# Optimization experiments

Measured on AMD Instinct MI355X. Metric: run time of the kernel, lower is better.

The kernel has to match this reference:

```python
import jax, jax.numpy as jnp
import numpy as np

T, B = 128, 256
WD, TD, RD, M = 300, 64, 64, 512
G = 5 * M  # 5 gates: i, f_down, f_left, o, u


def setup_inputs() -> dict:
    key = jax.random.key(0)
    ks = jax.random.split(key, 13)
    s = 0.05  # weight scale for numerical sanity
    return {
        "word": jax.random.normal(ks[0], (T, B, WD), jnp.float32),
        "tag": jax.random.normal(ks[1], (T, B, TD), jnp.float32),
        "rel": jax.random.normal(ks[2], (T, B, RD), jnp.float32),
        "k": jax.random.normal(ks[3], (T, B, M), jnp.float32),
        "q": jax.random.normal(ks[4], (T, B, M), jnp.float32),
        "h0": jnp.zeros((B, M), jnp.float32),
        "c0": jnp.zeros((B, M), jnp.float32),
        "Ww": jax.random.normal(ks[5], (WD, G), jnp.float32) * s,
        "Wt": jax.random.normal(ks[6], (TD, G), jnp.float32) * s,
        "Wr": jax.random.normal(ks[7], (RD, G), jnp.float32) * s,
        "Wk": jax.random.normal(ks[8], (M, G), jnp.float32) * s,
        "Wh": jax.random.normal(ks[9], (M, G), jnp.float32) * s,
        "b": jax.random.normal(ks[10], (G,), jnp.float32) * s,
    }


def reference(word, tag, rel, k, q, h0, c0, Ww, Wt, Wr, Wk, Wh, b):
    mem = h0.shape[-1]
    # Fuse all non-recurrent projections for all 5 gates into one pass:
    # [T,B,5M] preactivations from word/tag/rel/k (the per-child inputs).
    xp = (jnp.einsum('tbd,dg->tbg', word, Ww)
          + jnp.einsum('tbd,dg->tbg', tag, Wt)
          + jnp.einsum('tbd,dg->tbg', rel, Wr)
          + jnp.einsum('tbd,dg->tbg', k, Wk)
          + b)

    def step(carry, inp):
        h, c = carry
        xpt, qt = inp  # [B,5M], [B,M]
        g = xpt + h @ Wh
        gi, gfd, gfl, go, gu = (g[..., 0*mem:1*mem], g[..., 1*mem:2*mem],
                                g[..., 2*mem:3*mem], g[..., 3*mem:4*mem],
                                g[..., 4*mem:5*mem])
        i_ = jax.nn.sigmoid(gi)
        f_down = jax.nn.sigmoid(gfd)
        f_left = jax.nn.sigmoid(gfl)
        o_ = jax.nn.sigmoid(go)
        u_ = jnp.tanh(gu)
        c_new = i_ * u_ + f_down * qt + f_left * c
        h_new = o_ * jnp.tanh(c_new)
        return (h_new, c_new), None

    (h, c), _ = jax.lax.scan(step, (h0, c0), (xp, q))
    # node_forward returns (k, q) = (h, c) after consuming all children
    return jnp.concatenate([h, c], axis=-1)  # [B, 2*M]
```

## Files before the change

kernel.cpp:

```cpp
#include <hip/hip_runtime.h>
#include <hip/hip_bf16.h>

#define TT   128
#define BB   256
#define MM   512
#define GG   2560
#define K1P  960

typedef __attribute__((ext_vector_type(8))) short bf16x8;
typedef __attribute__((ext_vector_type(4))) short bf16x4;
typedef __attribute__((ext_vector_type(4))) float f32x4;
typedef __attribute__((ext_vector_type(4))) unsigned u32x4;

__device__ __forceinline__ float bf2f(unsigned short u){
  union { unsigned u; float f; } v; v.u = ((unsigned)u) << 16; return v.f;
}
__device__ __forceinline__ unsigned short f2bf(float f){
  union { float f; unsigned u; } v; v.f = f;
  unsigned r = v.u + 0x7fffu + ((v.u >> 16) & 1u);
  return (unsigned short)(r >> 16);
}
__device__ __forceinline__ float sigmoidf_(float x){ return 1.f/(1.f + __expf(-x)); }
__device__ __forceinline__ float tanhf_(float x){
  x = fminf(15.f, fmaxf(-15.f, x));
  float e = __expf(2.f*x);
  return (e - 1.f)/(e + 1.f);
}

__device__ __forceinline__ bf16x8 load_coh16b(const void* p){
  bf16x8 r;
  asm volatile("global_load_dwordx4 %0, %1, off sc0 sc1" : "=v"(r) : "v"(p) : "memory");
  return r;
}
__device__ __forceinline__ void store_coh4(void* p, unsigned v){
  asm volatile("global_store_dword %0, %1, off sc0 sc1" :: "v"(p), "v"(v) : "memory");
}

__device__ __forceinline__ void gll16(const unsigned short* g, unsigned short* l){
  __builtin_amdgcn_global_load_lds(
      (const __attribute__((address_space(1))) void*)(g),
      (__attribute__((address_space(3))) void*)(l),
      16, 0, 0);
}


__global__ __launch_bounds__(256) void stage_a(const float* __restrict__ word,
                                               const float* __restrict__ tag,
                                               const float* __restrict__ rel,
                                               const float* __restrict__ kin,
                                               unsigned short* __restrict__ A){
  long id = (long)blockIdx.x * 256 + threadIdx.x;
  int row = (int)(id / 120);
  int c8  = (int)(id % 120) * 8;
  bf16x8 o;
  #pragma unroll
  for (int j = 0; j < 8; ++j){
    int col = c8 + j; float v;
    if      (col < 300) v = word[(long)row*300 + col];
    else if (col < 364) v = tag [(long)row*64  + col-300];
    else if (col < 428) v = rel [(long)row*64  + col-364];
    else if (col < 940) v = kin [(long)row*512 + col-428];
    else v = 0.f;
    o[j] = (short)f2bf(v);
  }
  *reinterpret_cast<bf16x8*>(A + (long)row*K1P + c8) = o;
}

__global__ __launch_bounds__(256) void stage_wt(const float* __restrict__ Ww,
                                                const float* __restrict__ Wt,
                                                const float* __restrict__ Wr,
                                                const float* __restrict__ Wk,
                                                unsigned short* __restrict__ WT){
  long id = (long)blockIdx.x * 256 + threadIdx.x;
  int kk = (int)(id % K1P);
  int n  = (int)(id / K1P);
  float v;
  if      (kk < 300) v = Ww[(long)kk*GG + n];
  else if (kk < 364) v = Wt[(long)(kk-300)*GG + n];
  else if (kk < 428) v = Wr[(long)(kk-364)*GG + n];
  else if (kk < 940) v = Wk[(long)(kk-428)*GG + n];
  else v = 0.f;
  WT[(long)n*K1P + kk] = f2bf(v);
}

__global__ __launch_bounds__(256) void stage_wht(const float* __restrict__ Wh,
                                                 unsigned short* __restrict__ WhT){
  long id = (long)blockIdx.x * 256 + threadIdx.x;
  int kk = (int)(id % MM);
  int n  = (int)(id / MM);
  WhT[(long)n*MM + kk] = f2bf(Wh[(long)kk*GG + n]);
}

__global__ __launch_bounds__(256) void init_h(const float* __restrict__ h0,
                                              unsigned short* __restrict__ hb){
  int id = blockIdx.x * 256 + threadIdx.x;
  hb[id] = f2bf(h0[id]);
}

__global__ __launch_bounds__(256) void gemm_xp(const unsigned short* __restrict__ A,
                                               const unsigned short* __restrict__ WT,
                                               const float* __restrict__ bias,
                                               unsigned short* __restrict__ XP){
  __shared__ unsigned short As[128*32];
  __shared__ unsigned short Bs[128*32];
  const int tid  = threadIdx.x;
  const int wave = tid >> 6, lane = tid & 63;
  const int wr   = wave >> 1, wc = wave & 1;
  const int lrow = lane & 15, lhi = lane >> 4;
  const long row0 = (long)blockIdx.x * 128;
  const long col0 = (long)blockIdx.y * 128;

  const int sr0 = (wave*2 + 0)*16 + (lane >> 2);
  const int sr1 = (wave*2 + 1)*16 + (lane >> 2);
  const int sk  = (lane & 3) * 8;
  const unsigned short* ga0 = A  + (row0 + sr0)*K1P + sk;
  const unsigned short* ga1 = A  + (row0 + sr1)*K1P + sk;
  const unsigned short* gb0 = WT + (col0 + sr0)*K1P + sk;
  const unsigned short* gb1 = WT + (col0 + sr1)*K1P + sk;
  unsigned short* lA0 = As + (wave*2 + 0)*512;
  unsigned short* lA1 = As + (wave*2 + 1)*512;
  unsigned short* lB0 = Bs + (wave*2 + 0)*512;
  unsigned short* lB1 = Bs + (wave*2 + 1)*512;

  f32x4 acc[4][4] = {};
  for (int ks = 0; ks < 30; ++ks){
    const int k0 = ks * 32;
    __syncthreads();
    gll16(ga0 + k0, lA0);
    gll16(ga1 + k0, lA1);
    gll16(gb0 + k0, lB0);
    gll16(gb1 + k0, lB1);
    __syncthreads();
    bf16x8 af[4], bfr[4];
    #pragma unroll
    for (int mi = 0; mi < 4; ++mi)
      af[mi] = *reinterpret_cast<const bf16x8*>(As + (wr*64 + mi*16 + lrow)*32 + lhi*8);
    #pragma unroll
    for (int ni = 0; ni < 4; ++ni)
      bfr[ni] = *reinterpret_cast<const bf16x8*>(Bs + (wc*64 + ni*16 + lrow)*32 + lhi*8);
    #pragma unroll
    for (int mi = 0; mi < 4; ++mi)
      #pragma unroll
      for (int ni = 0; ni < 4; ++ni)
        acc[mi][ni] = __builtin_amdgcn_mfma_f32_16x16x32_bf16(af[mi], bfr[ni], acc[mi][ni], 0, 0, 0);
  }
  const int t     = (int)(row0 >> 8);
  const int brow0 = (int)(row0 & 255);
  #pragma unroll
  for (int ni = 0; ni < 4; ++ni){
    const int col = (int)col0 + wc*64 + ni*16 + lrow;
    const float bv = bias[col];
    #pragma unroll
    for (int mi = 0; mi < 4; ++mi){
      const int b4 = brow0 + wr*64 + mi*16 + lhi*4;
      bf16x4 pk;
      #pragma unroll
      for (int j = 0; j < 4; ++j) pk[j] = (short)f2bf(acc[mi][ni][j] + bv);
      *reinterpret_cast<bf16x4*>(XP + ((long)t*GG + col)*BB + b4) = pk;
    }
  }
}

__global__ __launch_bounds__(256, 1) void lstm_fused(const unsigned short* __restrict__ XP,
                                                     const float* __restrict__ q,
                                                     const unsigned short* __restrict__ WhT,
                                                     const float* __restrict__ c0,
                                                     unsigned short* __restrict__ hb0,
                                                     unsigned short* __restrict__ hb1,
                                                     float* __restrict__ out,
                                                     unsigned* __restrict__ cnts){
  __shared__ float Part[4][5][2][16][20];
  const int tid  = threadIdx.x;
  const int w    = tid >> 6, lane = tid & 63;
  const int lrow = lane & 15, lhi = lane >> 4;
  const int bt = blockIdx.x >> 5, mc = blockIdx.x & 31;
  const int b0 = bt * 32, m0 = mc * 16;
  unsigned* cnt = cnts + bt * 64;

  bf16x8 Breg[5][4];
  #pragma unroll
  for (int g = 0; g < 5; ++g)
    #pragma unroll
    for (int kf = 0; kf < 4; ++kf)
      Breg[g][kf] = *reinterpret_cast<const bf16x8*>(
          WhT + (long)(g*MM + m0 + lrow)*MM + w*128 + kf*32 + lhi*8);

  const int bl = tid >> 3, mi2 = (tid & 7) * 2;
  const int rt2 = bl >> 4, brow = bl & 15;
  const int gb = b0 + bl, gm = m0 + mi2;
  float cx = c0[(long)gb*MM + gm];
  float cy = c0[(long)gb*MM + gm + 1];

  unsigned short xv[5][2]; float qx, qy;
  #pragma unroll
  for (int j = 0; j < 5; ++j){
    xv[j][0] = XP[((long)0*GG + j*MM + gm    )*BB + gb];
    xv[j][1] = XP[((long)0*GG + j*MM + gm + 1)*BB + gb];
  }
  qx = q[((long)0*BB + gb)*MM + gm];
  qy = q[((long)0*BB + gb)*MM + gm + 1];

  for (int t = 0; t < TT; ++t){
    const unsigned short* hc = (t & 1) ? hb1 : hb0;
    unsigned short*       hn = (t & 1) ? hb0 : hb1;

    bf16x8 af[2][4];
    #pragma unroll
    for (int kf = 0; kf < 4; ++kf)
      #pragma unroll
      for (int rt = 0; rt < 2; ++rt)
        af[rt][kf] = load_coh16b(hc + (long)(b0 + rt*16 + lrow)*MM + w*128 + kf*32 + lhi*8);

    f32x4 acc[5][2] = {};
    #pragma unroll
    for (int kf = 0; kf < 4; ++kf){
      __builtin_amdgcn_sched_barrier(0);
      if      (kf == 0) asm volatile("s_waitcnt vmcnt(6)" ::: "memory");
      else if (kf == 1) asm volatile("s_waitcnt vmcnt(4)" ::: "memory");
      else if (kf == 2) asm volatile("s_waitcnt vmcnt(2)" ::: "memory");
      else              asm volatile("s_waitcnt vmcnt(0)" ::: "memory");
      __builtin_amdgcn_sched_barrier(0);
      #pragma unroll
      for (int rt = 0; rt < 2; ++rt)
        #pragma unroll
        for (int g = 0; g < 5; ++g)
          acc[g][rt] = __builtin_amdgcn_mfma_f32_16x16x32_bf16(af[rt][kf], Breg[g][kf], acc[g][rt], 0, 0, 0);
    }

    #pragma unroll
    for (int g = 0; g < 5; ++g)
      #pragma unroll
      for (int rt = 0; rt < 2; ++rt)
        *reinterpret_cast<f32x4*>(&Part[w][g][rt][lrow][lhi*4]) = acc[g][rt];
    __syncthreads();

    float gv[5][2];
    #pragma unroll
    for (int g = 0; g < 5; ++g)
      #pragma unroll
      for (int x = 0; x < 2; ++x)
        gv[g][x] = Part[0][g][rt2][mi2+x][brow] + Part[1][g][rt2][mi2+x][brow]
                 + Part[2][g][rt2][mi2+x][brow] + Part[3][g][rt2][mi2+x][brow]
                 + bf2f(xv[g][x]);
    const float qx_t = qx, qy_t = qy;

    if (t < TT - 1){
      #pragma unroll
      for (int j = 0; j < 5; ++j){
        xv[j][0] = XP[((long)(t+1)*GG + j*MM + gm    )*BB + gb];
        xv[j][1] = XP[((long)(t+1)*GG + j*MM + gm + 1)*BB + gb];
      }
      qx = q[((long)(t+1)*BB + gb)*MM + gm];
      qy = q[((long)(t+1)*BB + gb)*MM + gm + 1];
    }

    float hx, hy;
    {
      const float i_ = sigmoidf_(gv[0][0]);
      const float fd = sigmoidf_(gv[1][0]);
      const float fl = sigmoidf_(gv[2][0]);
      const float o_ = sigmoidf_(gv[3][0]);
      const float u_ = tanhf_(gv[4][0]);
      const float cn = i_*u_ + fd*qx_t + fl*cx;
      cx = cn; hx = o_*tanhf_(cn);
    }
    {
      const float i_ = sigmoidf_(gv[0][1]);
      const float fd = sigmoidf_(gv[1][1]);
      const float fl = sigmoidf_(gv[2][1]);
      const float o_ = sigmoidf_(gv[3][1]);
      const float u_ = tanhf_(gv[4][1]);
      const float cn = i_*u_ + fd*qy_t + fl*cy;
      cy = cn; hy = o_*tanhf_(cn);
    }
    const unsigned hv = (unsigned)f2bf(hx) | ((unsigned)f2bf(hy) << 16);
    store_coh4(hn + (long)gb*MM + gm, hv);
    if (t == TT - 1){
      out[(long)gb*1024 + gm]           = hx;
      out[(long)gb*1024 + gm + 1]       = hy;
      out[(long)gb*1024 + 512 + gm]     = cx;
      out[(long)gb*1024 + 512 + gm + 1] = cy;
    }

    if (t != TT - 1){
      __syncthreads();
      if (tid == 0){
        __hip_atomic_fetch_add(cnt, 1u, __ATOMIC_RELAXED, __HIP_MEMORY_SCOPE_AGENT);
        const unsigned target = (unsigned)(t + 1) * 32u;
        unsigned spins = 0;
        while (__hip_atomic_load(cnt, __ATOMIC_RELAXED, __HIP_MEMORY_SCOPE_AGENT) < target){
          __builtin_amdgcn_s_sleep(1);
          if (++spins > (1u << 20)) break;
        }
      }
      __syncthreads();
    }
  }
}

extern "C" void kernel_launch(void* const* d_in, const int* in_sizes, int n_in,
                              void* d_out, int out_size, void* d_ws, size_t ws_size,
                              hipStream_t stream){
  (void)in_sizes; (void)n_in; (void)out_size; (void)ws_size;
  const float* word = (const float*)d_in[0];
  const float* tag  = (const float*)d_in[1];
  const float* rel  = (const float*)d_in[2];
  const float* kin  = (const float*)d_in[3];
  const float* q    = (const float*)d_in[4];
  const float* h0   = (const float*)d_in[5];
  const float* c0   = (const float*)d_in[6];
  const float* Ww   = (const float*)d_in[7];
  const float* Wt   = (const float*)d_in[8];
  const float* Wr   = (const float*)d_in[9];
  const float* Wk   = (const float*)d_in[10];
  const float* Wh   = (const float*)d_in[11];
  const float* bias = (const float*)d_in[12];
  float* out = (float*)d_out;

  char* ws = (char*)d_ws;
  size_t off = 0;
  auto alloc = [&](size_t bytes)->void*{
    void* p = ws + off; off = (off + bytes + 255) & ~(size_t)255; return p;
  };
  unsigned short* Abf = (unsigned short*)alloc((size_t)TT*BB*K1P*2);
  unsigned short* WT  = (unsigned short*)alloc((size_t)GG*K1P*2);
  unsigned short* WhT = (unsigned short*)alloc((size_t)GG*MM*2);
  unsigned short* XP  = (unsigned short*)alloc((size_t)TT*BB*GG*2);
  unsigned short* hb0 = (unsigned short*)alloc((size_t)BB*MM*2);
  unsigned short* hb1 = (unsigned short*)alloc((size_t)BB*MM*2);
  unsigned*       cnt = (unsigned*)alloc(8 * 64 * sizeof(unsigned));

  hipMemsetAsync(cnt, 0, 8 * 64 * sizeof(unsigned), stream);

  stage_a  <<<dim3((TT*BB*(K1P/8) + 255)/256), 256, 0, stream>>>(word, tag, rel, kin, Abf);
  stage_wt <<<dim3((GG*K1P + 255)/256),        256, 0, stream>>>(Ww, Wt, Wr, Wk, WT);
  stage_wht<<<dim3((GG*MM + 255)/256),         256, 0, stream>>>(Wh, WhT);
  init_h   <<<dim3((BB*MM + 255)/256),         256, 0, stream>>>(h0, hb0);

  gemm_xp<<<dim3(TT*BB/128, GG/128), 256, 0, stream>>>(Abf, WT, bias, XP);

  lstm_fused<<<dim3(256), 256, 0, stream>>>(XP, q, WhT, c0, hb0, hb1, out, cnt);
}
```

Baseline: 849.6 us.

## Replace per-step counter barrier with step-tagged hidden-state words polled by consumers

The hidden state is now stored as 32-bit words that pack a bf16 value with a step tag in the upper half, double-buffered by step parity. Consumers spin-load their needed h fragments until every tag matches the current step. This removes the atomic counter barrier and its two block-wide syncs per step, so blocks wait only on the data they actually read. In exchange it doubles the bytes loaded and stored per h element, adds repacking ALU work, and re-issues the full load set on every spin iteration.

```diff
diff --git a/kernel.cpp b/kernel.cpp
--- a/kernel.cpp
+++ b/kernel.cpp
@@ -11,6 +11,7 @@
 typedef __attribute__((ext_vector_type(4))) short bf16x4;
 typedef __attribute__((ext_vector_type(4))) float f32x4;
 typedef __attribute__((ext_vector_type(4))) unsigned u32x4;
+typedef __attribute__((ext_vector_type(2))) unsigned u32x2;
 
 __device__ __forceinline__ float bf2f(unsigned short u){
   union { unsigned u; float f; } v; v.u = ((unsigned)u) << 16; return v.f;
@@ -27,13 +28,13 @@
   return (e - 1.f)/(e + 1.f);
 }
 
-__device__ __forceinline__ bf16x8 load_coh16b(const void* p){
-  bf16x8 r;
+__device__ __forceinline__ u32x4 load_coh16u(const void* p){
+  u32x4 r;
   asm volatile("global_load_dwordx4 %0, %1, off sc0 sc1" : "=v"(r) : "v"(p) : "memory");
   return r;
 }
-__device__ __forceinline__ void store_coh4(void* p, unsigned v){
-  asm volatile("global_store_dword %0, %1, off sc0 sc1" :: "v"(p), "v"(v) : "memory");
+__device__ __forceinline__ void store_coh8(void* p, u32x2 v){
+  asm volatile("global_store_dwordx2 %0, %1, off sc0 sc1" :: "v"(p), "v"(v) : "memory");
 }
 
 __device__ __forceinline__ void gll16(const unsigned short* g, unsigned short* l){
@@ -92,9 +93,9 @@
 }
 
 __global__ __launch_bounds__(256) void init_h(const float* __restrict__ h0,
-                                              unsigned short* __restrict__ hb){
+                                              unsigned* __restrict__ arr0){
   int id = blockIdx.x * 256 + threadIdx.x;
-  hb[id] = f2bf(h0[id]);
+  arr0[id] = (1u << 16) | (unsigned)f2bf(h0[id]);
 }
 
 __global__ __launch_bounds__(256) void gemm_xp(const unsigned short* __restrict__ A,
@@ -165,17 +166,14 @@
                                                      const float* __restrict__ q,
                                                      const unsigned short* __restrict__ WhT,
                                                      const float* __restrict__ c0,
-                                                     unsigned short* __restrict__ hb0,
-                                                     unsigned short* __restrict__ hb1,
-                                                     float* __restrict__ out,
-                                                     unsigned* __restrict__ cnts){
+                                                     unsigned* __restrict__ harr,
+                                                     float* __restrict__ out){
   __shared__ float Part[4][5][2][16][20];
   const int tid  = threadIdx.x;
   const int w    = tid >> 6, lane = tid & 63;
   const int lrow = lane & 15, lhi = lane >> 4;
   const int bt = blockIdx.x >> 5, mc = blockIdx.x & 31;
   const int b0 = bt * 32, m0 = mc * 16;
-  unsigned* cnt = cnts + bt * 64;
 
   bf16x8 Breg[5][4];
   #pragma unroll
@@ -201,31 +199,57 @@
   qy = q[((long)0*BB + gb)*MM + gm + 1];
 
   for (int t = 0; t < TT; ++t){
-    const unsigned short* hc = (t & 1) ? hb1 : hb0;
-    unsigned short*       hn = (t & 1) ? hb0 : hb1;
-
+    const unsigned* hb = harr + (size_t)(t & 1) * (BB*MM);
+    const unsigned etag = (unsigned)(t + 1);
+    u32x4 tv[2][4][2];
+    {
+      unsigned spins = 0;
+      for (;;){
+        #pragma unroll
+        for (int rt = 0; rt < 2; ++rt)
+          #pragma unroll
+          for (int kf = 0; kf < 4; ++kf){
+            const unsigned* p = hb + (b0 + rt*16 + lrow)*MM + w*128 + kf*32 + lhi*8;
+            tv[rt][kf][0] = load_coh16u(p);
+            tv[rt][kf][1] = load_coh16u(p + 4);
+          }
+        asm volatile("s_waitcnt vmcnt(0)" ::: "memory");
+        __builtin_amdgcn_sched_barrier(0);
+        unsigned diff = 0;
+        #pragma unroll
+        for (int rt = 0; rt < 2; ++rt)
+          #pragma unroll
+          for (int kf = 0; kf < 4; ++kf)
+            #pragma unroll
+            for (int h2 = 0; h2 < 2; ++h2){
+              diff |= (tv[rt][kf][h2][0] >> 16) ^ etag;
+              diff |= (tv[rt][kf][h2][2] >> 16) ^ etag;
+            }
+        if (diff == 0) break;
+        if (++spins > (1u << 16)) break;
+      }
+    }
     bf16x8 af[2][4];
     #pragma unroll
+    for (int rt = 0; rt < 2; ++rt)
+      #pragma unroll
+      for (int kf = 0; kf < 4; ++kf){
+        union { bf16x8 v; unsigned u[4]; } uu;
+        uu.u[0] = (tv[rt][kf][0][0] & 0xffffu) | (tv[rt][kf][0][1] << 16);
+        uu.u[1] = (tv[rt][kf][0][2] & 0xffffu) | (tv[rt][kf][0][3] << 16);
+        uu.u[2] = (tv[rt][kf][1][0] & 0xffffu) | (tv[rt][kf][1][1] << 16);
+        uu.u[3] = (tv[rt][kf][1][2] & 0xffffu) | (tv[rt][kf][1][3] << 16);
+        af[rt][kf] = uu.v;
+      }
+
+    f32x4 acc[5][2] = {};
+    #pragma unroll
     for (int kf = 0; kf < 4; ++kf)
-      #pragma unroll
-      for (int rt = 0; rt < 2; ++rt)
-        af[rt][kf] = load_coh16b(hc + (long)(b0 + rt*16 + lrow)*MM + w*128 + kf*32 + lhi*8);
-
-    f32x4 acc[5][2] = {};
-    #pragma unroll
-    for (int kf = 0; kf < 4; ++kf){
-      __builtin_amdgcn_sched_barrier(0);
-      if      (kf == 0) asm volatile("s_waitcnt vmcnt(6)" ::: "memory");
-      else if (kf == 1) asm volatile("s_waitcnt vmcnt(4)" ::: "memory");
-      else if (kf == 2) asm volatile("s_waitcnt vmcnt(2)" ::: "memory");
-      else              asm volatile("s_waitcnt vmcnt(0)" ::: "memory");
-      __builtin_amdgcn_sched_barrier(0);
       #pragma unroll
       for (int rt = 0; rt < 2; ++rt)
         #pragma unroll
         for (int g = 0; g < 5; ++g)
           acc[g][rt] = __builtin_amdgcn_mfma_f32_16x16x32_bf16(af[rt][kf], Breg[g][kf], acc[g][rt], 0, 0, 0);
-    }
 
     #pragma unroll
     for (int g = 0; g < 5; ++g)
@@ -243,6 +267,8 @@
                  + Part[2][g][rt2][mi2+x][brow] + Part[3][g][rt2][mi2+x][brow]
                  + bf2f(xv[g][x]);
     const float qx_t = qx, qy_t = qy;
+
+    __syncthreads();
 
     if (t < TT - 1){
       #pragma unroll
@@ -273,27 +299,19 @@
       const float cn = i_*u_ + fd*qy_t + fl*cy;
       cy = cn; hy = o_*tanhf_(cn);
     }
-    const unsigned hv = (unsigned)f2bf(hx) | ((unsigned)f2bf(hy) << 16);
-    store_coh4(hn + (long)gb*MM + gm, hv);
-    if (t == TT - 1){
+
+    if (t < TT - 1){
+      unsigned* nb = harr + (size_t)((t + 1) & 1) * (BB*MM);
+      const unsigned tg = (unsigned)(t + 2) << 16;
+      u32x2 pv;
+      pv[0] = tg | (unsigned)f2bf(hx);
+      pv[1] = tg | (unsigned)f2bf(hy);
+      store_coh8(nb + (long)gb*MM + gm, pv);
+    } else {
       out[(long)gb*1024 + gm]           = hx;
       out[(long)gb*1024 + gm + 1]       = hy;
       out[(long)gb*1024 + 512 + gm]     = cx;
       out[(long)gb*1024 + 512 + gm + 1] = cy;
-    }
-
-    if (t != TT - 1){
-      __syncthreads();
-      if (tid == 0){
-        __hip_atomic_fetch_add(cnt, 1u, __ATOMIC_RELAXED, __HIP_MEMORY_SCOPE_AGENT);
-        const unsigned target = (unsigned)(t + 1) * 32u;
-        unsigned spins = 0;
-        while (__hip_atomic_load(cnt, __ATOMIC_RELAXED, __HIP_MEMORY_SCOPE_AGENT) < target){
-          __builtin_amdgcn_s_sleep(1);
-          if (++spins > (1u << 20)) break;
-        }
-      }
-      __syncthreads();
     }
   }
 }
@@ -326,18 +344,16 @@
   unsigned short* WT  = (unsigned short*)alloc((size_t)GG*K1P*2);
   unsigned short* WhT = (unsigned short*)alloc((size_t)GG*MM*2);
   unsigned short* XP  = (unsigned short*)alloc((size_t)TT*BB*GG*2);
-  unsigned short* hb0 = (unsigned short*)alloc((size_t)BB*MM*2);
-  unsigned short* hb1 = (unsigned short*)alloc((size_t)BB*MM*2);
-  unsigned*       cnt = (unsigned*)alloc(8 * 64 * sizeof(unsigned));
-
-  hipMemsetAsync(cnt, 0, 8 * 64 * sizeof(unsigned), stream);
+  unsigned*       harr= (unsigned*)alloc((size_t)2*BB*MM*4);
+
+  hipMemsetAsync(harr, 0, (size_t)2*BB*MM*4, stream);
 
   stage_a  <<<dim3((TT*BB*(K1P/8) + 255)/256), 256, 0, stream>>>(word, tag, rel, kin, Abf);
   stage_wt <<<dim3((GG*K1P + 255)/256),        256, 0, stream>>>(Ww, Wt, Wr, Wk, WT);
   stage_wht<<<dim3((GG*MM + 255)/256),         256, 0, stream>>>(Wh, WhT);
-  init_h   <<<dim3((BB*MM + 255)/256),         256, 0, stream>>>(h0, hb0);
+  init_h   <<<dim3((BB*MM + 255)/256),         256, 0, stream>>>(h0, harr);
 
   gemm_xp<<<dim3(TT*BB/128, GG/128), 256, 0, stream>>>(Abf, WT, bias, XP);
 
-  lstm_fused<<<dim3(256), 256, 0, stream>>>(XP, q, WhT, c0, hb0, hb1, out, cnt);
-}
+  lstm_fused<<<dim3(256), 256, 0, stream>>>(XP, q, WhT, c0, harr, out);
+}
```

New measurement: 939.0 us. +10.5%, slower.

## Remap LSTM blocks by XCC and use cheaper coherence when groups share an XCC

Applied to the files above, without the earlier changes.

Changes the block-to-tile mapping so each batch group's 32 blocks are interleaved across block IDs, likely landing on one XCC under round-robin dispatch. At startup each block records its hardware XCC ID, and a per-group registration barrier checks whether the whole group shares one XCC. If so, h loads and stores use sc0-only (XCC-level) coherence instead of sc0 sc1 (device-level), which should cut latency on the per-step recurrent exchange. It also moves the next-step XP/q prefetch after the h store and polls the counter with explicit coherent loads. The gain relies on the dispatch-to-XCC assumption and adds a small startup barrier.

```diff
diff --git a/kernel.cpp b/kernel.cpp
--- a/kernel.cpp
+++ b/kernel.cpp
@@ -10,7 +10,6 @@
 typedef __attribute__((ext_vector_type(8))) short bf16x8;
 typedef __attribute__((ext_vector_type(4))) short bf16x4;
 typedef __attribute__((ext_vector_type(4))) float f32x4;
-typedef __attribute__((ext_vector_type(4))) unsigned u32x4;
 
 __device__ __forceinline__ float bf2f(unsigned short u){
   union { unsigned u; float f; } v; v.u = ((unsigned)u) << 16; return v.f;
@@ -27,12 +26,29 @@
   return (e - 1.f)/(e + 1.f);
 }
 
-__device__ __forceinline__ bf16x8 load_coh16b(const void* p){
+__device__ __forceinline__ void store_coh4(void* p, unsigned v){
+  asm volatile("global_store_dword %0, %1, off sc0 sc1" :: "v"(p), "v"(v) : "memory");
+}
+__device__ __forceinline__ unsigned load_coh_u32(const unsigned* p){
+  unsigned r;
+  asm volatile("global_load_dword %0, %1, off sc0 sc1" : "=v"(r) : "v"(p) : "memory");
+  asm volatile("s_waitcnt vmcnt(0)" ::: "memory");
+  return r;
+}
+__device__ __forceinline__ bf16x8 load_h16_f(const void* p){
+  bf16x8 r;
+  asm volatile("global_load_dwordx4 %0, %1, off sc0" : "=v"(r) : "v"(p) : "memory");
+  return r;
+}
+__device__ __forceinline__ bf16x8 load_h16_s(const void* p){
   bf16x8 r;
   asm volatile("global_load_dwordx4 %0, %1, off sc0 sc1" : "=v"(r) : "v"(p) : "memory");
   return r;
 }
-__device__ __forceinline__ void store_coh4(void* p, unsigned v){
+__device__ __forceinline__ void store_h32_f(void* p, unsigned v){
+  asm volatile("global_store_dword %0, %1, off sc0" :: "v"(p), "v"(v) : "memory");
+}
+__device__ __forceinline__ void store_h32_s(void* p, unsigned v){
   asm volatile("global_store_dword %0, %1, off sc0 sc1" :: "v"(p), "v"(v) : "memory");
 }
 
@@ -168,14 +184,32 @@
                                                      unsigned short* __restrict__ hb0,
                                                      unsigned short* __restrict__ hb1,
                                                      float* __restrict__ out,
-                                                     unsigned* __restrict__ cnts){
+                                                     unsigned* __restrict__ sync){
   __shared__ float Part[4][5][2][16][20];
   const int tid  = threadIdx.x;
   const int w    = tid >> 6, lane = tid & 63;
   const int lrow = lane & 15, lhi = lane >> 4;
-  const int bt = blockIdx.x >> 5, mc = blockIdx.x & 31;
+  const int bt = blockIdx.x & 7, mc = blockIdx.x >> 3;
   const int b0 = bt * 32, m0 = mc * 16;
-  unsigned* cnt = cnts + bt * 64;
+  unsigned* cnt    = sync + bt * 64;
+  unsigned* regcnt = sync + 512 + bt * 64;
+  unsigned* xccmap = sync + 1024;
+
+  unsigned xcc;
+  asm volatile("s_getreg_b32 %0, hwreg(HW_REG_XCC_ID)" : "=s"(xcc));
+  if (tid == 0){
+    store_coh4(xccmap + blockIdx.x, xcc);
+    asm volatile("s_waitcnt vmcnt(0)" ::: "memory");
+    __hip_atomic_fetch_add(regcnt, 1u, __ATOMIC_RELAXED, __HIP_MEMORY_SCOPE_AGENT);
+    unsigned spins = 0;
+    while (load_coh_u32(regcnt) < 32u){
+      __builtin_amdgcn_s_sleep(1);
+      if (++spins > (1u << 16)) break;
+    }
+  }
+  __syncthreads();
+  unsigned mj = (lane < 32) ? load_coh_u32(xccmap + bt + 8*(lane & 31)) : xcc;
+  const bool fast = (__ballot(mj == xcc) == ~0ull);
 
   bf16x8 Breg[5][4];
   #pragma unroll
@@ -205,11 +239,19 @@
     unsigned short*       hn = (t & 1) ? hb0 : hb1;
 
     bf16x8 af[2][4];
-    #pragma unroll
-    for (int kf = 0; kf < 4; ++kf)
-      #pragma unroll
-      for (int rt = 0; rt < 2; ++rt)
-        af[rt][kf] = load_coh16b(hc + (long)(b0 + rt*16 + lrow)*MM + w*128 + kf*32 + lhi*8);
+    if (fast){
+      #pragma unroll
+      for (int kf = 0; kf < 4; ++kf)
+        #pragma unroll
+        for (int rt = 0; rt < 2; ++rt)
+          af[rt][kf] = load_h16_f(hc + (long)(b0 + rt*16 + lrow)*MM + w*128 + kf*32 + lhi*8);
+    } else {
+      #pragma unroll
+      for (int kf = 0; kf < 4; ++kf)
+        #pragma unroll
+        for (int rt = 0; rt < 2; ++rt)
+          af[rt][kf] = load_h16_s(hc + (long)(b0 + rt*16 + lrow)*MM + w*128 + kf*32 + lhi*8);
+    }
 
     f32x4 acc[5][2] = {};
     #pragma unroll
@@ -242,17 +284,6 @@
         gv[g][x] = Part[0][g][rt2][mi2+x][brow] + Part[1][g][rt2][mi2+x][brow]
                  + Part[2][g][rt2][mi2+x][brow] + Part[3][g][rt2][mi2+x][brow]
                  + bf2f(xv[g][x]);
-    const float qx_t = qx, qy_t = qy;
-
-    if (t < TT - 1){
-      #pragma unroll
-      for (int j = 0; j < 5; ++j){
-        xv[j][0] = XP[((long)(t+1)*GG + j*MM + gm    )*BB + gb];
-        xv[j][1] = XP[((long)(t+1)*GG + j*MM + gm + 1)*BB + gb];
-      }
-      qx = q[((long)(t+1)*BB + gb)*MM + gm];
-      qy = q[((long)(t+1)*BB + gb)*MM + gm + 1];
-    }
 
     float hx, hy;
     {
@@ -261,7 +292,7 @@
       const float fl = sigmoidf_(gv[2][0]);
       const float o_ = sigmoidf_(gv[3][0]);
       const float u_ = tanhf_(gv[4][0]);
-      const float cn = i_*u_ + fd*qx_t + fl*cx;
+      const float cn = i_*u_ + fd*qx + fl*cx;
       cx = cn; hx = o_*tanhf_(cn);
     }
     {
@@ -270,16 +301,29 @@
       const float fl = sigmoidf_(gv[2][1]);
       const float o_ = sigmoidf_(gv[3][1]);
       const float u_ = tanhf_(gv[4][1]);
-      const float cn = i_*u_ + fd*qy_t + fl*cy;
+      const float cn = i_*u_ + fd*qy + fl*cy;
       cy = cn; hy = o_*tanhf_(cn);
     }
+
     const unsigned hv = (unsigned)f2bf(hx) | ((unsigned)f2bf(hy) << 16);
-    store_coh4(hn + (long)gb*MM + gm, hv);
-    if (t == TT - 1){
+    if (t < TT - 1){
+      if (fast) store_h32_f(hn + (long)gb*MM + gm, hv);
+      else      store_h32_s(hn + (long)gb*MM + gm, hv);
+    } else {
       out[(long)gb*1024 + gm]           = hx;
       out[(long)gb*1024 + gm + 1]       = hy;
       out[(long)gb*1024 + 512 + gm]     = cx;
       out[(long)gb*1024 + 512 + gm + 1] = cy;
+    }
+
+    if (t < TT - 1){
+      #pragma unroll
+      for (int j = 0; j < 5; ++j){
+        xv[j][0] = XP[((long)(t+1)*GG + j*MM + gm    )*BB + gb];
+        xv[j][1] = XP[((long)(t+1)*GG + j*MM + gm + 1)*BB + gb];
+      }
+      qx = q[((long)(t+1)*BB + gb)*MM + gm];
+      qy = q[((long)(t+1)*BB + gb)*MM + gm + 1];
     }
 
     if (t != TT - 1){
@@ -288,7 +332,7 @@
         __hip_atomic_fetch_add(cnt, 1u, __ATOMIC_RELAXED, __HIP_MEMORY_SCOPE_AGENT);
         const unsigned target = (unsigned)(t + 1) * 32u;
         unsigned spins = 0;
-        while (__hip_atomic_load(cnt, __ATOMIC_RELAXED, __HIP_MEMORY_SCOPE_AGENT) < target){
+        while (load_coh_u32(cnt) < target){
           __builtin_amdgcn_s_sleep(1);
           if (++spins > (1u << 20)) break;
         }
@@ -328,9 +372,9 @@
   unsigned short* XP  = (unsigned short*)alloc((size_t)TT*BB*GG*2);
   unsigned short* hb0 = (unsigned short*)alloc((size_t)BB*MM*2);
   unsigned short* hb1 = (unsigned short*)alloc((size_t)BB*MM*2);
-  unsigned*       cnt = (unsigned*)alloc(8 * 64 * sizeof(unsigned));
-
-  hipMemsetAsync(cnt, 0, 8 * 64 * sizeof(unsigned), stream);
+  unsigned*       syn = (unsigned*)alloc((size_t)(512 + 512 + 256)*4);
+
+  hipMemsetAsync(syn, 0, (size_t)(512 + 512 + 256)*4, stream);
 
   stage_a  <<<dim3((TT*BB*(K1P/8) + 255)/256), 256, 0, stream>>>(word, tag, rel, kin, Abf);
   stage_wt <<<dim3((GG*K1P + 255)/256),        256, 0, stream>>>(Ww, Wt, Wr, Wk, WT);
@@ -339,5 +383,5 @@
 
   gemm_xp<<<dim3(TT*BB/128, GG/128), 256, 0, stream>>>(Abf, WT, bias, XP);
 
-  lstm_fused<<<dim3(256), 256, 0, stream>>>(XP, q, WhT, c0, hb0, hb1, out, cnt);
-}
+  lstm_fused<<<dim3(256), 256, 0, stream>>>(XP, q, WhT, c0, hb0, hb1, out, syn);
+}
```

Result: faster. 739.1 us (-13.0%).

## Widen GEMM K-tile with XOR-swizzled LDS, remap blocks, and reorder LSTM loads

Applied to the files above, without the earlier changes.

The projection GEMM now uses a 64-wide K tile with an XOR-swizzled LDS layout and a 1D grid whose block index is remapped for cache locality. This halves the number of barrier iterations and is meant to avoid LDS bank conflicts. In the recurrent kernel, the next-step XP and q prefetches move after the gate math and h store, and addressing uses precomputed offsets. The barrier spin-wait now uses a coherent inline-asm load. These changes risk lower occupancy from the doubled LDS and change when load latency is exposed before the barrier.

```diff
diff --git a/kernel.cpp b/kernel.cpp
--- a/kernel.cpp
+++ b/kernel.cpp
@@ -10,7 +10,6 @@
 typedef __attribute__((ext_vector_type(8))) short bf16x8;
 typedef __attribute__((ext_vector_type(4))) short bf16x4;
 typedef __attribute__((ext_vector_type(4))) float f32x4;
-typedef __attribute__((ext_vector_type(4))) unsigned u32x4;
 
 __device__ __forceinline__ float bf2f(unsigned short u){
   union { unsigned u; float f; } v; v.u = ((unsigned)u) << 16; return v.f;
@@ -27,12 +26,21 @@
   return (e - 1.f)/(e + 1.f);
 }
 
-__device__ __forceinline__ bf16x8 load_coh16b(const void* p){
+__device__ __forceinline__ void store_coh4(void* p, unsigned v){
+  asm volatile("global_store_dword %0, %1, off sc0 sc1" :: "v"(p), "v"(v) : "memory");
+}
+__device__ __forceinline__ unsigned load_coh_u32(const unsigned* p){
+  unsigned r;
+  asm volatile("global_load_dword %0, %1, off sc0 sc1" : "=v"(r) : "v"(p) : "memory");
+  asm volatile("s_waitcnt vmcnt(0)" ::: "memory");
+  return r;
+}
+__device__ __forceinline__ bf16x8 load_h16(const void* p){
   bf16x8 r;
   asm volatile("global_load_dwordx4 %0, %1, off sc0 sc1" : "=v"(r) : "v"(p) : "memory");
   return r;
 }
-__device__ __forceinline__ void store_coh4(void* p, unsigned v){
+__device__ __forceinline__ void store_h32(void* p, unsigned v){
   asm volatile("global_store_dword %0, %1, off sc0 sc1" :: "v"(p), "v"(v) : "memory");
 }
 
@@ -101,48 +109,52 @@
                                                const unsigned short* __restrict__ WT,
                                                const float* __restrict__ bias,
                                                unsigned short* __restrict__ XP){
-  __shared__ unsigned short As[128*32];
-  __shared__ unsigned short Bs[128*32];
+  __shared__ unsigned short As[128*64];
+  __shared__ unsigned short Bs[128*64];
   const int tid  = threadIdx.x;
   const int wave = tid >> 6, lane = tid & 63;
   const int wr   = wave >> 1, wc = wave & 1;
   const int lrow = lane & 15, lhi = lane >> 4;
-  const long row0 = (long)blockIdx.x * 128;
-  const long col0 = (long)blockIdx.y * 128;
-
-  const int sr0 = (wave*2 + 0)*16 + (lane >> 2);
-  const int sr1 = (wave*2 + 1)*16 + (lane >> 2);
-  const int sk  = (lane & 3) * 8;
-  const unsigned short* ga0 = A  + (row0 + sr0)*K1P + sk;
-  const unsigned short* ga1 = A  + (row0 + sr1)*K1P + sk;
-  const unsigned short* gb0 = WT + (col0 + sr0)*K1P + sk;
-  const unsigned short* gb1 = WT + (col0 + sr1)*K1P + sk;
-  unsigned short* lA0 = As + (wave*2 + 0)*512;
-  unsigned short* lA1 = As + (wave*2 + 1)*512;
-  unsigned short* lB0 = Bs + (wave*2 + 0)*512;
-  unsigned short* lB1 = Bs + (wave*2 + 1)*512;
+
+  const int swz = (blockIdx.x & 7) * (5120 / 8) + (blockIdx.x >> 3);
+  const long row0 = (long)(swz & 255) * 128;
+  const long col0 = (long)(swz >> 8) * 128;
+
+  const int srow = wave*8 + (lane >> 3);
+  const int scol = (((lane & 7) ^ (lane >> 3)) * 8);
+  const unsigned short* gaB = A  + (row0 + srow)*K1P + scol;
+  const unsigned short* gbB = WT + (col0 + srow)*K1P + scol;
 
   f32x4 acc[4][4] = {};
-  for (int ks = 0; ks < 30; ++ks){
-    const int k0 = ks * 32;
+  for (int ks = 0; ks < 15; ++ks){
+    const int k0 = ks * 64;
     __syncthreads();
-    gll16(ga0 + k0, lA0);
-    gll16(ga1 + k0, lA1);
-    gll16(gb0 + k0, lB0);
-    gll16(gb1 + k0, lB1);
+    #pragma unroll
+    for (int s = 0; s < 4; ++s){
+      gll16(gaB + (long)s*32*K1P + k0, As + (s*32 + wave*8)*64);
+      gll16(gbB + (long)s*32*K1P + k0, Bs + (s*32 + wave*8)*64);
+    }
     __syncthreads();
-    bf16x8 af[4], bfr[4];
-    #pragma unroll
-    for (int mi = 0; mi < 4; ++mi)
-      af[mi] = *reinterpret_cast<const bf16x8*>(As + (wr*64 + mi*16 + lrow)*32 + lhi*8);
-    #pragma unroll
-    for (int ni = 0; ni < 4; ++ni)
-      bfr[ni] = *reinterpret_cast<const bf16x8*>(Bs + (wc*64 + ni*16 + lrow)*32 + lhi*8);
-    #pragma unroll
-    for (int mi = 0; mi < 4; ++mi)
+    bf16x8 af[2][4], bfr[2][4];
+    const int sx = (lrow & 7) * 8;
+    #pragma unroll
+    for (int kk = 0; kk < 2; ++kk){
+      #pragma unroll
+      for (int mi = 0; mi < 4; ++mi)
+        af[kk][mi] = *reinterpret_cast<const bf16x8*>(
+            As + (wr*64 + mi*16 + lrow)*64 + ((kk*32 + lhi*8) ^ sx));
       #pragma unroll
       for (int ni = 0; ni < 4; ++ni)
-        acc[mi][ni] = __builtin_amdgcn_mfma_f32_16x16x32_bf16(af[mi], bfr[ni], acc[mi][ni], 0, 0, 0);
+        bfr[kk][ni] = *reinterpret_cast<const bf16x8*>(
+            Bs + (wc*64 + ni*16 + lrow)*64 + ((kk*32 + lhi*8) ^ sx));
+    }
+    #pragma unroll
+    for (int kk = 0; kk < 2; ++kk)
+      #pragma unroll
+      for (int mi = 0; mi < 4; ++mi)
+        #pragma unroll
+        for (int ni = 0; ni < 4; ++ni)
+          acc[mi][ni] = __builtin_amdgcn_mfma_f32_16x16x32_bf16(af[kk][mi], bfr[kk][ni], acc[mi][ni], 0, 0, 0);
   }
   const int t     = (int)(row0 >> 8);
   const int brow0 = (int)(row0 & 255);
@@ -191,14 +203,21 @@
   float cx = c0[(long)gb*MM + gm];
   float cy = c0[(long)gb*MM + gm + 1];
 
+  long oj[5];
+  #pragma unroll
+  for (int j = 0; j < 5; ++j) oj[j] = ((long)j*MM + gm)*BB + gb;
+  const long qb0 = (long)gb*MM + gm;
+  const long XSTEP = (long)GG*BB, QSTEP = (long)BB*MM;
+
   unsigned short xv[5][2]; float qx, qy;
   #pragma unroll
   for (int j = 0; j < 5; ++j){
-    xv[j][0] = XP[((long)0*GG + j*MM + gm    )*BB + gb];
-    xv[j][1] = XP[((long)0*GG + j*MM + gm + 1)*BB + gb];
-  }
-  qx = q[((long)0*BB + gb)*MM + gm];
-  qy = q[((long)0*BB + gb)*MM + gm + 1];
+    xv[j][0] = XP[oj[j]];
+    xv[j][1] = XP[oj[j] + BB];
+  }
+  qx = q[qb0];
+  qy = q[qb0 + 1];
+  long xo = XSTEP, qo = QSTEP;
 
   for (int t = 0; t < TT; ++t){
     const unsigned short* hc = (t & 1) ? hb1 : hb0;
@@ -209,7 +228,7 @@
     for (int kf = 0; kf < 4; ++kf)
       #pragma unroll
       for (int rt = 0; rt < 2; ++rt)
-        af[rt][kf] = load_coh16b(hc + (long)(b0 + rt*16 + lrow)*MM + w*128 + kf*32 + lhi*8);
+        af[rt][kf] = load_h16(hc + (long)(b0 + rt*16 + lrow)*MM + w*128 + kf*32 + lhi*8);
 
     f32x4 acc[5][2] = {};
     #pragma unroll
@@ -242,17 +261,6 @@
         gv[g][x] = Part[0][g][rt2][mi2+x][brow] + Part[1][g][rt2][mi2+x][brow]
                  + Part[2][g][rt2][mi2+x][brow] + Part[3][g][rt2][mi2+x][brow]
                  + bf2f(xv[g][x]);
-    const float qx_t = qx, qy_t = qy;
-
-    if (t < TT - 1){
-      #pragma unroll
-      for (int j = 0; j < 5; ++j){
-        xv[j][0] = XP[((long)(t+1)*GG + j*MM + gm    )*BB + gb];
-        xv[j][1] = XP[((long)(t+1)*GG + j*MM + gm + 1)*BB + gb];
-      }
-      qx = q[((long)(t+1)*BB + gb)*MM + gm];
-      qy = q[((long)(t+1)*BB + gb)*MM + gm + 1];
-    }
 
     float hx, hy;
     {
@@ -261,7 +269,7 @@
       const float fl = sigmoidf_(gv[2][0]);
       const float o_ = sigmoidf_(gv[3][0]);
       const float u_ = tanhf_(gv[4][0]);
-      const float cn = i_*u_ + fd*qx_t + fl*cx;
+      const float cn = i_*u_ + fd*qx + fl*cx;
       cx = cn; hx = o_*tanhf_(cn);
     }
     {
@@ -270,16 +278,29 @@
       const float fl = sigmoidf_(gv[2][1]);
       const float o_ = sigmoidf_(gv[3][1]);
       const float u_ = tanhf_(gv[4][1]);
-      const float cn = i_*u_ + fd*qy_t + fl*cy;
+      const float cn = i_*u_ + fd*qy + fl*cy;
       cy = cn; hy = o_*tanhf_(cn);
     }
+
     const unsigned hv = (unsigned)f2bf(hx) | ((unsigned)f2bf(hy) << 16);
-    store_coh4(hn + (long)gb*MM + gm, hv);
-    if (t == TT - 1){
+    if (t < TT - 1){
+      store_h32(hn + (long)gb*MM + gm, hv);
+    } else {
       out[(long)gb*1024 + gm]           = hx;
       out[(long)gb*1024 + gm + 1]       = hy;
       out[(long)gb*1024 + 512 + gm]     = cx;
       out[(long)gb*1024 + 512 + gm + 1] = cy;
+    }
+
+    if (t < TT - 1){
+      #pragma unroll
+      for (int j = 0; j < 5; ++j){
+        xv[j][0] = XP[xo + oj[j]];
+        xv[j][1] = XP[xo + oj[j] + BB];
+      }
+      qx = q[qo + qb0];
+      qy = q[qo + qb0 + 1];
+      xo += XSTEP; qo += QSTEP;
     }
 
     if (t != TT - 1){
@@ -288,7 +309,7 @@
         __hip_atomic_fetch_add(cnt, 1u, __ATOMIC_RELAXED, __HIP_MEMORY_SCOPE_AGENT);
         const unsigned target = (unsigned)(t + 1) * 32u;
         unsigned spins = 0;
-        while (__hip_atomic_load(cnt, __ATOMIC_RELAXED, __HIP_MEMORY_SCOPE_AGENT) < target){
+        while (load_coh_u32(cnt) < target){
           __builtin_amdgcn_s_sleep(1);
           if (++spins > (1u << 20)) break;
         }
@@ -337,7 +358,7 @@
   stage_wht<<<dim3((GG*MM + 255)/256),         256, 0, stream>>>(Wh, WhT);
   init_h   <<<dim3((BB*MM + 255)/256),         256, 0, stream>>>(h0, hb0);
 
-  gemm_xp<<<dim3(TT*BB/128, GG/128), 256, 0, stream>>>(Abf, WT, bias, XP);
+  gemm_xp<<<dim3(5120), 256, 0, stream>>>(Abf, WT, bias, XP);
 
   lstm_fused<<<dim3(256), 256, 0, stream>>>(XP, q, WhT, c0, hb0, hb1, out, cnt);
 }
```

New measurement: 773.1 us. -9.0%, faster.
